# Kernel optimization log

Hardware: AMD Instinct MI355X
Metric: run time of the kernel (lower is better)

Reference implementation:

```python
import jax, jax.numpy as jnp
import numpy as np

B = 1024        # num samples
D = 1024        # feature dim d = DIM * K_RANK
K_RANK = 16     # data_object.k (low rank)
DIM = 64        # d / k
N_CLASSES = 10
L = 16          # residual layers


def setup_inputs() -> dict:
    key = jax.random.key(0)
    ks = jax.random.split(key, 7)
    X = jax.random.normal(ks[0], (B, 3, D), jnp.float32)
    W0 = jax.random.normal(ks[1], (D, D), jnp.float32) / np.sqrt(D).astype(np.float32)
    Ws = jax.random.normal(ks[2], (L, D, D), jnp.float32) / np.sqrt(D).astype(np.float32)
    bs = jax.random.normal(ks[3], (L, D), jnp.float32) * 0.01
    Wc = jax.random.normal(ks[4], (N_CLASSES, DIM * DIM), jnp.float32) / np.sqrt(DIM * DIM).astype(np.float32)
    bc = jax.random.normal(ks[5], (N_CLASSES,), jnp.float32) * 0.01
    h = jnp.full((1,), 1.0 / L, jnp.float32)  # trainable stepsize, init 1/L
    return {"X": X, "h": h, "W0": W0, "Ws": Ws, "bs": bs, "Wc": Wc, "bc": bc}


def _polar(A):
    # polar projection onto Stiefel: U[:, :, :k] @ Vh[:, :k, :] == reduced U @ Vh
    U, S, Vh = jnp.linalg.svd(A, full_matrices=False)
    return U @ Vh


def _project_svd(X):
    # X: (B, 3, D); channels = (U_tilde, S, V_tilde), each matrix is (DIM, K_RANK)
    U = _polar(X[:, 0].reshape(-1, DIM, K_RANK))
    V = _polar(X[:, 2].reshape(-1, DIM, K_RANK))
    return jnp.stack([U.reshape(-1, D), X[:, 1], V.reshape(-1, D)], axis=1)


def reference(X, h, W0, Ws, bs, Wc, bc):
    # preprocessing: vh stored row-major as (k, dim) -> v = vh^T flattened
    v = jnp.swapaxes(X[:, 2].reshape(-1, K_RANK, DIM), 1, 2).reshape(-1, D)
    X = jnp.stack([X[:, 0], X[:, 1], v], axis=1)  # (B, 3, D)

    # layer 0: Linear without bias, then Stiefel projection
    X = _project_svd(jnp.einsum('bcd,ed->bce', X, W0))
    xs = [X]

    # residual layers: X <- Proj(X + h * relu(Linear(X)))
    for i in range(L):
        Y = X + h[0] * jax.nn.relu(jnp.einsum('bcd,ed->bce', X, Ws[i]) + bs[i])
        X = _project_svd(Y)
        xs.append(X)

    X_transformed = jnp.stack(xs, axis=-1)  # (B, 3, D, L+1)

    # reconstruct: U @ S[:k,:k] @ V^T, then classify
    U = X[:, 0].reshape(-1, DIM, K_RANK)
    S = X[:, 1].reshape(-1, DIM, K_RANK)[:, :K_RANK, :K_RANK]
    V = X[:, 2].reshape(-1, DIM, K_RANK)
    Z = (U @ S @ jnp.swapaxes(V, 1, 2)).reshape(-1, DIM * DIM)
    X_classified = Z @ Wc.T + bc
    X_predicted = jax.nn.softmax(X_classified, axis=1)
    return X_predicted, X_classified, X_transformed
```

## Files before the change

### kernel.cpp

```cpp
#include <hip/hip_runtime.h>
#include <hip/hip_bf16.h>

#define DD    1024
#define NROWS 3072
#define NLAY  17
#define MS    20

typedef __attribute__((ext_vector_type(8))) short short8;
typedef __attribute__((ext_vector_type(4))) float floatx4;

__global__ __launch_bounds__(256) void convw_kernel(const float* __restrict__ W0,
                                                    const float* __restrict__ Ws,
                                                    ushort* __restrict__ Wbf) {
  const size_t i4 = ((size_t)blockIdx.x * 256 + threadIdx.x) * 4;
  float4 v;
  if (i4 < 1048576) v = *(const float4*)(W0 + i4);
  else              v = *(const float4*)(Ws + (i4 - 1048576));
  union { __hip_bfloat16 h[4]; ushort u[4]; } pk;
  pk.h[0] = __float2bfloat16(v.x); pk.h[1] = __float2bfloat16(v.y);
  pk.h[2] = __float2bfloat16(v.z); pk.h[3] = __float2bfloat16(v.w);
  *(ushort4*)(Wbf + i4) = *(ushort4*)pk.u;
}

__global__ __launch_bounds__(256) void prep_kernel(const float* __restrict__ Xin,
                                                   ushort* __restrict__ X0bf) {
  const int row = blockIdx.x;
  const int c   = row % 3;
  const float* src = Xin + (size_t)row * DD;
  ushort* dst = X0bf + (size_t)row * DD;
  for (int t = threadIdx.x; t < DD; t += 256) {
    float v;
    if (c == 2) v = src[(t & 15) * 64 + (t >> 4)];
    else        v = src[t];
    __hip_bfloat16 h = __float2bfloat16(v);
    dst[t] = *(ushort*)&h;
  }
}

__global__ __launch_bounds__(256) void gemm_kernel(
    const ushort* __restrict__ Abf, const ushort* __restrict__ Wbf,
    const float* __restrict__ Xres, const float* __restrict__ bias,
    const float* __restrict__ hp, float* __restrict__ Y, int fuse)
{
  __shared__ __align__(16) ushort As[128 * 32];
  __shared__ __align__(16) ushort Bs[64 * 32];
  const int tid  = threadIdx.x;
  const int wave = tid >> 6, lane = tid & 63;

  const int id = blockIdx.x;
  const int w  = (id & 7) * 48 + (id >> 3);
  const int bm = (w >> 4) * 128;
  const int bn = (w & 15) * 64;

  const int srow = wave * 16 + (lane >> 2);
  const int scol = (lane & 3) * 8;
  const ushort* ga0 = Abf + (size_t)(bm + srow) * DD + scol;
  const ushort* gb0 = Wbf + (size_t)(bn + srow) * DD + scol;

  const int wm0 = (wave >> 1) * 64, wn0 = (wave & 1) * 32;
  const int m = lane & 15, quad = lane >> 4;

  floatx4 acc[4][2] = {};

  for (int k0 = 0; k0 < DD; k0 += 32) {
    __syncthreads();
#pragma unroll
    for (int q = 0; q < 2; ++q) {
      __builtin_amdgcn_global_load_lds(
          (const __attribute__((address_space(1))) unsigned int*)(ga0 + (size_t)q * 64 * DD + k0),
          (__attribute__((address_space(3))) unsigned int*)&As[(q * 64 + wave * 16) * 32],
          16, 0, 0);
    }
    __builtin_amdgcn_global_load_lds(
        (const __attribute__((address_space(1))) unsigned int*)(gb0 + k0),
        (__attribute__((address_space(3))) unsigned int*)&Bs[(wave * 16) * 32],
        16, 0, 0);
    __syncthreads();

    short8 av[4], bv[2];
#pragma unroll
    for (int i = 0; i < 4; ++i)
      av[i] = *(const short8*)&As[(wm0 + i * 16 + m) * 32 + quad * 8];
#pragma unroll
    for (int j = 0; j < 2; ++j)
      bv[j] = *(const short8*)&Bs[(wn0 + j * 16 + m) * 32 + quad * 8];
#pragma unroll
    for (int i = 0; i < 4; ++i)
#pragma unroll
      for (int j = 0; j < 2; ++j)
        acc[i][j] = __builtin_amdgcn_mfma_f32_16x16x32_bf16(av[i], bv[j], acc[i][j], 0, 0, 0);
  }

  const float h = fuse ? hp[0] : 0.0f;
#pragma unroll
  for (int i = 0; i < 4; ++i) {
#pragma unroll
    for (int r = 0; r < 4; ++r) {
      const int grow = bm + wm0 + i * 16 + quad * 4 + r;
      float* yr = Y + (size_t)grow * DD;
      const float* xr = Xres + (size_t)grow * DD;
#pragma unroll
      for (int j = 0; j < 2; ++j) {
        const int gcol = bn + wn0 + j * 16 + m;
        float d = acc[i][j][r];
        if (fuse) d = xr[gcol] + h * fmaxf(d + bias[gcol], 0.0f);
        yr[gcol] = d;
      }
    }
  }
}

__device__ __forceinline__ void split_wr(ushort* Bh, ushort* Bl, int c, int q, floatx4 a) {
  union { ushort u[4]; uint2 d; } ph, pl;
#pragma unroll
  for (int j = 0; j < 4; ++j) {
    const float x = a[j];
    __hip_bfloat16 hb = __float2bfloat16(x);
    const float hf = __bfloat162float(hb);
    __hip_bfloat16 lb = __float2bfloat16(x - hf);
    ph.u[j] = *(const ushort*)&hb;
    pl.u[j] = *(const ushort*)&lb;
  }
  *(uint2*)&Bh[c * 40 + q * 4] = ph.d;
  *(uint2*)&Bl[c * 40 + q * 4] = pl.d;
}

__global__ __launch_bounds__(64) void proj_kernel(
    const float* __restrict__ Yg, float* __restrict__ Xg,
    __hip_bfloat16* __restrict__ stage, int layer, int iters)
{
  __shared__ __align__(16) ushort POOL[5632];

  const int lane = threadIdx.x;

  if (blockIdx.x >= 2048) {
    const int b = blockIdx.x - 2048;
    const int row = b * 3 + 1;
    const float* src = Yg + (size_t)row * DD + lane * 16;
    float* dst = Xg + (size_t)row * DD + lane * 16;
    float v[16];
#pragma unroll
    for (int q = 0; q < 4; ++q) {
      const float4 t4 = *(const float4*)(src + q * 4);
      v[q*4+0]=t4.x; v[q*4+1]=t4.y; v[q*4+2]=t4.z; v[q*4+3]=t4.w;
      *(float4*)(dst + q * 4) = t4;
    }
    union { __hip_bfloat16 hh[16]; uint4 u[2]; } pk;
#pragma unroll
    for (int j = 0; j < 16; ++j) pk.hh[j] = __float2bfloat16(v[j]);
    uint4* sd = (uint4*)(stage + ((size_t)layer * NROWS + row) * DD + lane * 16);
    sd[0] = pk.u[0]; sd[1] = pk.u[1];
    return;
  }

  const int p = blockIdx.x;
  const int b = p >> 1;
  const int row = b * 3 + (p & 1) * 2;
  const float* src = Yg + (size_t)row * DD + lane * 16;

  float v[16];
#pragma unroll
  for (int q = 0; q < 4; ++q) {
    const float4 t4 = *(const float4*)(src + q * 4);
    v[q*4+0]=t4.x; v[q*4+1]=t4.y; v[q*4+2]=t4.z; v[q*4+3]=t4.w;
  }
  float nrm = 0.f;
#pragma unroll
  for (int j = 0; j < 16; ++j) nrm += v[j] * v[j];
#pragma unroll
  for (int o = 32; o > 0; o >>= 1) nrm += __shfl_xor(nrm, o, 64);
  const float s = rsqrtf(nrm + 1e-30f);
#pragma unroll
  for (int j = 0; j < 16; ++j) v[j] *= s;

  ushort* ATl = POOL;
  ushort* Bh  = POOL + 1152;
  ushort* Bl  = POOL + 1792;
  const int fr = lane & 15, fq = lane >> 4;

#pragma unroll
  for (int j = 0; j < 16; ++j) {
    __hip_bfloat16 hb = __float2bfloat16(v[j]);
    ATl[j * 72 + lane] = *(const ushort*)&hb;
  }
  *(uint2*)&Bh[fr * 40 + 16 + fq * 4] = make_uint2(0u, 0u);
  *(uint2*)&Bl[fr * 40 + 16 + fq * 4] = make_uint2(0u, 0u);
  asm volatile("" ::: "memory");

  short8 g1 = *(const short8*)&ATl[fr * 72 + fq * 8];
  short8 g2 = *(const short8*)&ATl[fr * 72 + 32 + fq * 8];
  floatx4 gacc = {};
  gacc = __builtin_amdgcn_mfma_f32_16x16x32_bf16(g1, g1, gacc, 0, 0, 0);
  gacc = __builtin_amdgcn_mfma_f32_16x16x32_bf16(g2, g2, gacc, 0, 0, 0);

  float ss = gacc[0]*gacc[0] + gacc[1]*gacc[1] + gacc[2]*gacc[2] + gacc[3]*gacc[3];
#pragma unroll
  for (int o = 32; o > 0; o >>= 1) ss += __shfl_xor(ss, o, 64);
  const float gf = rsqrtf(ss + 1e-30f);

  floatx4 yd;
#pragma unroll
  for (int j = 0; j < 4; ++j) yd[j] = gacc[j] * gf;
  split_wr(Bh, Bl, fr, fq, yd);
  asm volatile("" ::: "memory");
  short8 Yh = *(const short8*)&Bh[fr * 40 + fq * 8];
  short8 Yl = *(const short8*)&Bl[fr * 40 + fq * 8];
  short8 Zh, Zl;
#pragma unroll
  for (int d = 0; d < 8; ++d) {
    Zh[d] = (fr == fq * 8 + d) ? (short)0x3F80 : (short)0;
    Zl[d] = 0;
  }

  for (int it = 0; it < iters; ++it) {
    floatx4 wv = {};
    wv = __builtin_amdgcn_mfma_f32_16x16x32_bf16(Zh, Yh, wv, 0, 0, 0);
    wv = __builtin_amdgcn_mfma_f32_16x16x32_bf16(Zh, Yl, wv, 0, 0, 0);
    wv = __builtin_amdgcn_mfma_f32_16x16x32_bf16(Zl, Yh, wv, 0, 0, 0);
    floatx4 td;
#pragma unroll
    for (int j = 0; j < 4; ++j)
      td[j] = ((fq * 4 + j == fr) ? 1.5f : 0.f) - 0.5f * wv[j];
    split_wr(Bh, Bl, fr, fq, td);
    asm volatile("" ::: "memory");
    short8 Th = *(const short8*)&Bh[fr * 40 + fq * 8];
    short8 Tl = *(const short8*)&Bl[fr * 40 + fq * 8];
    floatx4 zd = {};
    zd = __builtin_amdgcn_mfma_f32_16x16x32_bf16(Zh, Th, zd, 0, 0, 0);
    zd = __builtin_amdgcn_mfma_f32_16x16x32_bf16(Zh, Tl, zd, 0, 0, 0);
    zd = __builtin_amdgcn_mfma_f32_16x16x32_bf16(Zl, Th, zd, 0, 0, 0);
    if (it < iters - 1) {
      floatx4 yn = {};
      yn = __builtin_amdgcn_mfma_f32_16x16x32_bf16(Yh, Th, yn, 0, 0, 0);
      yn = __builtin_amdgcn_mfma_f32_16x16x32_bf16(Yh, Tl, yn, 0, 0, 0);
      yn = __builtin_amdgcn_mfma_f32_16x16x32_bf16(Yl, Th, yn, 0, 0, 0);
      split_wr(Bh, Bl, fr, fq, yn);
      asm volatile("" ::: "memory");
      Yh = *(const short8*)&Bh[fr * 40 + fq * 8];
      Yl = *(const short8*)&Bl[fr * 40 + fq * 8];
    }
    split_wr(Bh, Bl, fr, fq, zd);
    asm volatile("" ::: "memory");
    Zh = *(const short8*)&Bh[fr * 40 + fq * 8];
    Zl = *(const short8*)&Bl[fr * 40 + fq * 8];
  }

  const float us = sqrtf(gf);
  asm volatile("" ::: "memory");
  ushort* Ah = POOL;
  ushort* Al = POOL + 2560;
  {
    union { ushort u[16]; uint4 q4[2]; } rh, rl;
#pragma unroll
    for (int j = 0; j < 16; ++j) {
      const float x = v[j] * us;
      __hip_bfloat16 hb = __float2bfloat16(x);
      const float hf = __bfloat162float(hb);
      __hip_bfloat16 lb = __float2bfloat16(x - hf);
      rh.u[j] = *(const ushort*)&hb;
      rl.u[j] = *(const ushort*)&lb;
    }
    *(uint4*)&Ah[lane * 40]      = rh.q4[0];
    *(uint4*)&Ah[lane * 40 + 8]  = rh.q4[1];
    *(uint4*)&Al[lane * 40]      = rl.q4[0];
    *(uint4*)&Al[lane * 40 + 8]  = rl.q4[1];
    const uint4 zz = make_uint4(0u, 0u, 0u, 0u);
    *(uint4*)&Ah[lane * 40 + 16] = zz; *(uint4*)&Ah[lane * 40 + 24] = zz;
    *(uint4*)&Al[lane * 40 + 16] = zz; *(uint4*)&Al[lane * 40 + 24] = zz;
  }
  asm volatile("" ::: "memory");
  short8 ah[4], al[4];
#pragma unroll
  for (int m4 = 0; m4 < 4; ++m4) {
    ah[m4] = *(const short8*)&Ah[(m4 * 16 + fr) * 40 + fq * 8];
    al[m4] = *(const short8*)&Al[(m4 * 16 + fr) * 40 + fq * 8];
  }
  floatx4 um[4];
#pragma unroll
  for (int m4 = 0; m4 < 4; ++m4) {
    floatx4 a = {};
    a = __builtin_amdgcn_mfma_f32_16x16x32_bf16(ah[m4], Zh, a, 0, 0, 0);
    a = __builtin_amdgcn_mfma_f32_16x16x32_bf16(ah[m4], Zl, a, 0, 0, 0);
    a = __builtin_amdgcn_mfma_f32_16x16x32_bf16(al[m4], Zh, a, 0, 0, 0);
    um[m4] = a;
  }
  asm volatile("" ::: "memory");
  float* Ub = (float*)POOL;
#pragma unroll
  for (int m4 = 0; m4 < 4; ++m4)
#pragma unroll
    for (int j = 0; j < 4; ++j)
      Ub[(m4 * 16 + fq * 4 + j) * 20 + fr] = um[m4][j];
  asm volatile("" ::: "memory");
  float up[16];
#pragma unroll
  for (int i = 0; i < 4; ++i) {
    const float4 t4 = *(const float4*)&Ub[lane * 20 + i * 4];
    up[i*4+0]=t4.x; up[i*4+1]=t4.y; up[i*4+2]=t4.z; up[i*4+3]=t4.w;
  }
  float* dst = Xg + (size_t)row * DD + lane * 16;
#pragma unroll
  for (int q = 0; q < 4; ++q)
    *(float4*)(dst + q*4) = make_float4(up[q*4], up[q*4+1], up[q*4+2], up[q*4+3]);
  union { __hip_bfloat16 hh[16]; uint4 u[2]; } pk;
#pragma unroll
  for (int j = 0; j < 16; ++j) pk.hh[j] = __float2bfloat16(up[j]);
  uint4* sd = (uint4*)(stage + ((size_t)layer * NROWS + row) * DD + lane * 16);
  sd[0] = pk.u[0]; sd[1] = pk.u[1];
}

__global__ __launch_bounds__(256) void transpose_kernel(
    const __hip_bfloat16* __restrict__ stage, float* __restrict__ outT)
{
  __shared__ float buf[256 * 18];
  const int row = blockIdx.y;
  const int d0  = blockIdx.x * 256;
  const int t   = threadIdx.x;
  for (int l = 0; l < NLAY; ++l)
    buf[t * 18 + l] = __bfloat162float(stage[((size_t)l * NROWS + row) * DD + d0 + t]);
  __syncthreads();
  const size_t ob = (size_t)(row * DD + d0) * NLAY;
  for (int i = 0; i < NLAY; ++i) {
    const int idx = i * 256 + t;
    const int dd = idx / 17, ll = idx % 17;
    outT[ob + idx] = buf[dd * 18 + ll];
  }
}

__global__ __launch_bounds__(256) void classify_kernel(
    const float* __restrict__ X, const float* __restrict__ Wc,
    const float* __restrict__ bc, float* __restrict__ out)
{
  __shared__ float U[64*17], S[16*17], V[64*17], T[64*17];
  __shared__ float Z[4096];
  __shared__ float wsum[4][10];
  const int b = blockIdx.x, t = threadIdx.x;
  const float* x0 = X + (size_t)(b*3+0) * DD;
  const float* x1 = X + (size_t)(b*3+1) * DD;
  const float* x2 = X + (size_t)(b*3+2) * DD;
  for (int e = t; e < 1024; e += 256) {
    const int i = e >> 4, j = e & 15;
    U[i*17+j] = x0[e];
    V[i*17+j] = x2[e];
  }
  { const int i = t >> 4, j = t & 15; if (t < 256) S[i*17+j] = x1[i*16+j]; }
  __syncthreads();
  for (int e = t; e < 1024; e += 256) {
    const int i = e >> 4, j = e & 15;
    float a = 0.f;
    for (int k = 0; k < 16; ++k) a = fmaf(U[i*17+k], S[k*17+j], a);
    T[i*17+j] = a;
  }
  __syncthreads();
  for (int e = t; e < 4096; e += 256) {
    const int i = e >> 6, j = e & 63;
    float a = 0.f;
    for (int k = 0; k < 16; ++k) a = fmaf(T[i*17+k], V[j*17+k], a);
    Z[e] = a;
  }
  __syncthreads();
  float part[10] = {};
  for (int e = t; e < 4096; e += 256) {
    const float z = Z[e];
#pragma unroll
    for (int n = 0; n < 10; ++n) part[n] = fmaf(z, Wc[(size_t)n * 4096 + e], part[n]);
  }
#pragma unroll
  for (int n = 0; n < 10; ++n) {
#pragma unroll
    for (int off = 32; off > 0; off >>= 1) part[n] += __shfl_xor(part[n], off, 64);
  }
  if ((t & 63) == 0) {
#pragma unroll
    for (int n = 0; n < 10; ++n) wsum[t >> 6][n] = part[n];
  }
  __syncthreads();
  if (t == 0) {
    float logits[10];
#pragma unroll
    for (int n = 0; n < 10; ++n)
      logits[n] = wsum[0][n] + wsum[1][n] + wsum[2][n] + wsum[3][n] + bc[n];
    float mx = logits[0];
    for (int n = 1; n < 10; ++n) mx = fmaxf(mx, logits[n]);
    float ex[10], sm = 0.f;
    for (int n = 0; n < 10; ++n) { ex[n] = expf(logits[n] - mx); sm += ex[n]; }
    const float inv = 1.f / sm;
    for (int n = 0; n < 10; ++n) {
      out[b*10 + n] = ex[n] * inv;
      out[10240 + b*10 + n] = logits[n];
    }
  }
}

extern "C" void kernel_launch(void* const* d_in, const int* in_sizes, int n_in,
                              void* d_out, int out_size, void* d_ws, size_t ws_size,
                              hipStream_t stream) {
  const float* Xin = (const float*)d_in[0];
  const float* hp  = (const float*)d_in[1];
  const float* W0  = (const float*)d_in[2];
  const float* Ws  = (const float*)d_in[3];
  const float* bs  = (const float*)d_in[4];
  const float* Wc  = (const float*)d_in[5];
  const float* bc  = (const float*)d_in[6];
  float* out = (float*)d_out;

  char* ws = (char*)d_ws;
  float* Xb = (float*)ws;
  float* Yb = Xb + (size_t)NROWS * DD;
  __hip_bfloat16* stage =
      (__hip_bfloat16*)(ws + 2 * (size_t)NROWS * DD * 4);
  ushort* X0bf = (ushort*)(ws + 2 * (size_t)NROWS * DD * 4
                              + (size_t)NLAY * NROWS * DD * 2);
  ushort* Wbf  = X0bf + (size_t)NROWS * DD;

  convw_kernel<<<17408, 256, 0, stream>>>(W0, Ws, Wbf);
  prep_kernel<<<NROWS, 256, 0, stream>>>(Xin, X0bf);

  gemm_kernel<<<384, 256, 0, stream>>>(X0bf, Wbf, Xb, bs, hp, Yb, 0);
  proj_kernel<<<3072, 64, 0, stream>>>(Yb, Xb, stage, 0, 13);

  for (int l = 0; l < 16; ++l) {
    gemm_kernel<<<384, 256, 0, stream>>>(
        (const ushort*)(stage + (size_t)l * NROWS * DD),
        Wbf + (size_t)(l + 1) * DD * DD,
        Xb, bs + (size_t)l * DD, hp, Yb, 1);
    proj_kernel<<<3072, 64, 0, stream>>>(Yb, Xb, stage, l + 1, 9);
  }

  transpose_kernel<<<dim3(4, NROWS), 256, 0, stream>>>(stage, out + 20480);
  classify_kernel<<<1024, 256, 0, stream>>>(Xb, Wc, bc, out);
}
```

Baseline: 1.004 ms.

## Double-buffer GEMM with smaller 64x64 tiles and merge prologue/epilogue kernels

The GEMM tile shrinks from 128x64 to 64x64, which doubles the grid to 768 blocks, and the kernel now double-buffers LDS so the next k-slice loads while the current one computes. That leaves one barrier per iteration instead of two. The weight-conversion and input-prep kernels are merged into one launch, and so are the transpose and classify kernels, cutting two launches. In exchange, each block does less reuse per A/B tile load.

New measurement: 975.5 us. 1.03x faster.

```diff
diff --git a/kernel.cpp b/kernel.cpp
--- a/kernel.cpp
+++ b/kernel.cpp
@@ -4,27 +4,27 @@
 #define DD    1024
 #define NROWS 3072
 #define NLAY  17
-#define MS    20
 
 typedef __attribute__((ext_vector_type(8))) short short8;
 typedef __attribute__((ext_vector_type(4))) float floatx4;
 
-__global__ __launch_bounds__(256) void convw_kernel(const float* __restrict__ W0,
-                                                    const float* __restrict__ Ws,
-                                                    ushort* __restrict__ Wbf) {
-  const size_t i4 = ((size_t)blockIdx.x * 256 + threadIdx.x) * 4;
-  float4 v;
-  if (i4 < 1048576) v = *(const float4*)(W0 + i4);
-  else              v = *(const float4*)(Ws + (i4 - 1048576));
-  union { __hip_bfloat16 h[4]; ushort u[4]; } pk;
-  pk.h[0] = __float2bfloat16(v.x); pk.h[1] = __float2bfloat16(v.y);
-  pk.h[2] = __float2bfloat16(v.z); pk.h[3] = __float2bfloat16(v.w);
-  *(ushort4*)(Wbf + i4) = *(ushort4*)pk.u;
-}
-
-__global__ __launch_bounds__(256) void prep_kernel(const float* __restrict__ Xin,
-                                                   ushort* __restrict__ X0bf) {
-  const int row = blockIdx.x;
+__global__ __launch_bounds__(256) void convprep_kernel(
+    const float* __restrict__ W0, const float* __restrict__ Ws,
+    ushort* __restrict__ Wbf, const float* __restrict__ Xin,
+    ushort* __restrict__ X0bf)
+{
+  if (blockIdx.x < 17408) {
+    const size_t i4 = ((size_t)blockIdx.x * 256 + threadIdx.x) * 4;
+    float4 v;
+    if (i4 < 1048576) v = *(const float4*)(W0 + i4);
+    else              v = *(const float4*)(Ws + (i4 - 1048576));
+    union { __hip_bfloat16 h[4]; ushort u[4]; } pk;
+    pk.h[0] = __float2bfloat16(v.x); pk.h[1] = __float2bfloat16(v.y);
+    pk.h[2] = __float2bfloat16(v.z); pk.h[3] = __float2bfloat16(v.w);
+    *(ushort4*)(Wbf + i4) = *(ushort4*)pk.u;
+    return;
+  }
+  const int row = blockIdx.x - 17408;
   const int c   = row % 3;
   const float* src = Xin + (size_t)row * DD;
   ushort* dst = X0bf + (size_t)row * DD;
@@ -42,58 +42,77 @@
     const float* __restrict__ Xres, const float* __restrict__ bias,
     const float* __restrict__ hp, float* __restrict__ Y, int fuse)
 {
-  __shared__ __align__(16) ushort As[128 * 32];
-  __shared__ __align__(16) ushort Bs[64 * 32];
+  __shared__ __align__(16) ushort As[2][64 * 32];
+  __shared__ __align__(16) ushort Bs[2][64 * 32];
   const int tid  = threadIdx.x;
   const int wave = tid >> 6, lane = tid & 63;
 
   const int id = blockIdx.x;
-  const int w  = (id & 7) * 48 + (id >> 3);
-  const int bm = (w >> 4) * 128;
+  const int w  = (id & 7) * 96 + (id >> 3);
+  const int bm = (w >> 4) * 64;
   const int bn = (w & 15) * 64;
 
   const int srow = wave * 16 + (lane >> 2);
   const int scol = (lane & 3) * 8;
   const ushort* ga0 = Abf + (size_t)(bm + srow) * DD + scol;
   const ushort* gb0 = Wbf + (size_t)(bn + srow) * DD + scol;
-
-  const int wm0 = (wave >> 1) * 64, wn0 = (wave & 1) * 32;
+  const int sdst = (wave * 16) * 32;
+
+  const int wm0 = (wave >> 1) * 32, wn0 = (wave & 1) * 32;
   const int m = lane & 15, quad = lane >> 4;
 
-  floatx4 acc[4][2] = {};
-
-  for (int k0 = 0; k0 < DD; k0 += 32) {
-    __syncthreads();
-#pragma unroll
-    for (int q = 0; q < 2; ++q) {
-      __builtin_amdgcn_global_load_lds(
-          (const __attribute__((address_space(1))) unsigned int*)(ga0 + (size_t)q * 64 * DD + k0),
-          (__attribute__((address_space(3))) unsigned int*)&As[(q * 64 + wave * 16) * 32],
-          16, 0, 0);
-    }
+  floatx4 acc[2][2] = {};
+
+  __builtin_amdgcn_global_load_lds(
+      (const __attribute__((address_space(1))) unsigned int*)(ga0),
+      (__attribute__((address_space(3))) unsigned int*)&As[0][sdst], 16, 0, 0);
+  __builtin_amdgcn_global_load_lds(
+      (const __attribute__((address_space(1))) unsigned int*)(gb0),
+      (__attribute__((address_space(3))) unsigned int*)&Bs[0][sdst], 16, 0, 0);
+  __syncthreads();
+
+  int cur = 0;
+  for (int t = 0; t < 31; ++t) {
+    const int k1 = (t + 1) * 32;
     __builtin_amdgcn_global_load_lds(
-        (const __attribute__((address_space(1))) unsigned int*)(gb0 + k0),
-        (__attribute__((address_space(3))) unsigned int*)&Bs[(wave * 16) * 32],
-        16, 0, 0);
-    __syncthreads();
-
-    short8 av[4], bv[2];
-#pragma unroll
-    for (int i = 0; i < 4; ++i)
-      av[i] = *(const short8*)&As[(wm0 + i * 16 + m) * 32 + quad * 8];
+        (const __attribute__((address_space(1))) unsigned int*)(ga0 + k1),
+        (__attribute__((address_space(3))) unsigned int*)&As[cur ^ 1][sdst], 16, 0, 0);
+    __builtin_amdgcn_global_load_lds(
+        (const __attribute__((address_space(1))) unsigned int*)(gb0 + k1),
+        (__attribute__((address_space(3))) unsigned int*)&Bs[cur ^ 1][sdst], 16, 0, 0);
+    short8 av[2], bv[2];
+#pragma unroll
+    for (int i = 0; i < 2; ++i)
+      av[i] = *(const short8*)&As[cur][(wm0 + i * 16 + m) * 32 + quad * 8];
 #pragma unroll
     for (int j = 0; j < 2; ++j)
-      bv[j] = *(const short8*)&Bs[(wn0 + j * 16 + m) * 32 + quad * 8];
-#pragma unroll
-    for (int i = 0; i < 4; ++i)
+      bv[j] = *(const short8*)&Bs[cur][(wn0 + j * 16 + m) * 32 + quad * 8];
+#pragma unroll
+    for (int i = 0; i < 2; ++i)
 #pragma unroll
       for (int j = 0; j < 2; ++j)
         acc[i][j] = __builtin_amdgcn_mfma_f32_16x16x32_bf16(av[i], bv[j], acc[i][j], 0, 0, 0);
+    __syncthreads();
+    cur ^= 1;
+  }
+  {
+    short8 av[2], bv[2];
+#pragma unroll
+    for (int i = 0; i < 2; ++i)
+      av[i] = *(const short8*)&As[cur][(wm0 + i * 16 + m) * 32 + quad * 8];
+#pragma unroll
+    for (int j = 0; j < 2; ++j)
+      bv[j] = *(const short8*)&Bs[cur][(wn0 + j * 16 + m) * 32 + quad * 8];
+#pragma unroll
+    for (int i = 0; i < 2; ++i)
+#pragma unroll
+      for (int j = 0; j < 2; ++j)
+        acc[i][j] = __builtin_amdgcn_mfma_f32_16x16x32_bf16(av[i], bv[j], acc[i][j], 0, 0, 0);
   }
 
   const float h = fuse ? hp[0] : 0.0f;
 #pragma unroll
-  for (int i = 0; i < 4; ++i) {
+  for (int i = 0; i < 2; ++i) {
 #pragma unroll
     for (int r = 0; r < 4; ++r) {
       const int grow = bm + wm0 + i * 16 + quad * 4 + r;
@@ -309,32 +328,37 @@
   sd[0] = pk.u[0]; sd[1] = pk.u[1];
 }
 
-__global__ __launch_bounds__(256) void transpose_kernel(
-    const __hip_bfloat16* __restrict__ stage, float* __restrict__ outT)
-{
-  __shared__ float buf[256 * 18];
-  const int row = blockIdx.y;
-  const int d0  = blockIdx.x * 256;
-  const int t   = threadIdx.x;
-  for (int l = 0; l < NLAY; ++l)
-    buf[t * 18 + l] = __bfloat162float(stage[((size_t)l * NROWS + row) * DD + d0 + t]);
-  __syncthreads();
-  const size_t ob = (size_t)(row * DD + d0) * NLAY;
-  for (int i = 0; i < NLAY; ++i) {
-    const int idx = i * 256 + t;
-    const int dd = idx / 17, ll = idx % 17;
-    outT[ob + idx] = buf[dd * 18 + ll];
-  }
-}
-
-__global__ __launch_bounds__(256) void classify_kernel(
+__global__ __launch_bounds__(256) void tail_kernel(
+    const __hip_bfloat16* __restrict__ stage, float* __restrict__ outT,
     const float* __restrict__ X, const float* __restrict__ Wc,
     const float* __restrict__ bc, float* __restrict__ out)
 {
-  __shared__ float U[64*17], S[16*17], V[64*17], T[64*17];
-  __shared__ float Z[4096];
-  __shared__ float wsum[4][10];
-  const int b = blockIdx.x, t = threadIdx.x;
+  __shared__ __align__(16) float pool[7680];
+  const int t = threadIdx.x;
+
+  if (blockIdx.x < 12288) {
+    float* buf = pool;
+    const int row = blockIdx.x >> 2;
+    const int d0  = (blockIdx.x & 3) * 256;
+    for (int l = 0; l < NLAY; ++l)
+      buf[t * 18 + l] = __bfloat162float(stage[((size_t)l * NROWS + row) * DD + d0 + t]);
+    __syncthreads();
+    const size_t ob = (size_t)(row * DD + d0) * NLAY;
+    for (int i = 0; i < NLAY; ++i) {
+      const int idx = i * 256 + t;
+      const int dd = idx / 17, ll = idx % 17;
+      outT[ob + idx] = buf[dd * 18 + ll];
+    }
+    return;
+  }
+
+  const int b = blockIdx.x - 12288;
+  float* U = pool;
+  float* S = U + 1088;
+  float* V = S + 272;
+  float* T = V + 1088;
+  float* Z = T + 1088;
+  float* wsum = Z + 4096;
   const float* x0 = X + (size_t)(b*3+0) * DD;
   const float* x1 = X + (size_t)(b*3+1) * DD;
   const float* x2 = X + (size_t)(b*3+2) * DD;
@@ -372,14 +396,14 @@
   }
   if ((t & 63) == 0) {
 #pragma unroll
-    for (int n = 0; n < 10; ++n) wsum[t >> 6][n] = part[n];
+    for (int n = 0; n < 10; ++n) wsum[(t >> 6) * 10 + n] = part[n];
   }
   __syncthreads();
   if (t == 0) {
     float logits[10];
 #pragma unroll
     for (int n = 0; n < 10; ++n)
-      logits[n] = wsum[0][n] + wsum[1][n] + wsum[2][n] + wsum[3][n] + bc[n];
+      logits[n] = wsum[0*10+n] + wsum[1*10+n] + wsum[2*10+n] + wsum[3*10+n] + bc[n];
     float mx = logits[0];
     for (int n = 1; n < 10; ++n) mx = fmaxf(mx, logits[n]);
     float ex[10], sm = 0.f;
@@ -413,20 +437,18 @@
                               + (size_t)NLAY * NROWS * DD * 2);
   ushort* Wbf  = X0bf + (size_t)NROWS * DD;
 
-  convw_kernel<<<17408, 256, 0, stream>>>(W0, Ws, Wbf);
-  prep_kernel<<<NROWS, 256, 0, stream>>>(Xin, X0bf);
-
-  gemm_kernel<<<384, 256, 0, stream>>>(X0bf, Wbf, Xb, bs, hp, Yb, 0);
+  convprep_kernel<<<20480, 256, 0, stream>>>(W0, Ws, Wbf, Xin, X0bf);
+
+  gemm_kernel<<<768, 256, 0, stream>>>(X0bf, Wbf, Xb, bs, hp, Yb, 0);
   proj_kernel<<<3072, 64, 0, stream>>>(Yb, Xb, stage, 0, 13);
 
   for (int l = 0; l < 16; ++l) {
-    gemm_kernel<<<384, 256, 0, stream>>>(
+    gemm_kernel<<<768, 256, 0, stream>>>(
         (const ushort*)(stage + (size_t)l * NROWS * DD),
         Wbf + (size_t)(l + 1) * DD * DD,
         Xb, bs + (size_t)l * DD, hp, Yb, 1);
     proj_kernel<<<3072, 64, 0, stream>>>(Yb, Xb, stage, l + 1, 9);
   }
 
-  transpose_kernel<<<dim3(4, NROWS), 256, 0, stream>>>(stage, out + 20480);
-  classify_kernel<<<1024, 256, 0, stream>>>(Xb, Wc, bc, out);
-}
+  tail_kernel<<<13312, 256, 0, stream>>>(stage, out + 20480, Xb, Wc, bc, out);
+}
```
